# Kernel optimization log

Hardware: AMD Instinct MI355X
Metric: run time of the kernel (lower is better)

Reference implementation:

```python
import jax, jax.numpy as jnp
from jax import lax
import numpy as np

NH = 4                      # num_heads in CrossScaleCom
KS = [3, 5, 7, 9]           # per-head depthwise kernel sizes
WS = 2                      # window_size in LocalFeatureGuided
GGM_K = 7                   # guide-token generator kernel size


def _dwconv(x, w, stride, pad):
    # depthwise conv: w has shape (C, 1, k, k), feature_group_count = C
    return lax.conv_general_dilated(
        x, w, (stride, stride), [(pad, pad), (pad, pad)],
        feature_group_count=x.shape[1],
        dimension_numbers=("NCHW", "OIHW", "NCHW"))


def _forward(x, dw_w0, dw_b0, dw_w1, dw_b1, dw_w2, dw_b2, dw_w3, dw_b3,
             csc_w, csc_b, bn_gamma, bn_beta, bn_mean, bn_var,
             ggm_w, ggm_b, qkv_w, qkv_b, proj_w, proj_b):
    B, C, H, W = x.shape
    cph = C // NH
    # ---- CrossScaleCom: per-head multi-scale depthwise convs ----
    xh = x.reshape(B, NH, cph, H, W)
    dws = [(dw_w0, dw_b0), (dw_w1, dw_b1), (dw_w2, dw_b2), (dw_w3, dw_b3)]
    heads = [_dwconv(xh[:, i], w, 1, KS[i] // 2) + b[None, :, None, None]
             for i, (w, b) in enumerate(dws)]
    y = jnp.stack(heads, 1)                      # (B, NH, cph, H, W)
    y = y.transpose(0, 2, 1, 3, 4).reshape(B, C, H, W)  # channel shuffle
    y = jnp.einsum("bchw,oc->bohw", y, csc_w) + csc_b[None, :, None, None]
    Co = y.shape[1]
    # ---- LocalFeatureGuided ----
    # ggm: BatchNorm (eval) -> GELU (exact) -> depthwise conv k=7 stride=WS
    inv = bn_gamma / jnp.sqrt(bn_var + 1e-5)
    g = (y - bn_mean[None, :, None, None]) * inv[None, :, None, None] \
        + bn_beta[None, :, None, None]
    g = jax.nn.gelu(g, approximate=False)
    g = _dwconv(g, ggm_w, WS, GGM_K // 2) + ggm_b[None, :, None, None]  # (B,Co,Ho,Wo)
    Ho, Wo = H // WS, W // WS
    L = Ho * Wo
    # unfold(kernel=WS, stride=WS) -> (B, Co, WS*WS, L), torch unfold ordering
    xu = y.reshape(B, Co, Ho, WS, Wo, WS).transpose(0, 1, 3, 5, 2, 4)
    xu = xu.reshape(B, Co, WS * WS, L)
    tokens = jnp.concatenate([g.reshape(B, Co, 1, L), xu], axis=2)  # (B,Co,5,L)
    # 1x1 conv over channel dim == einsum
    qkv = jnp.einsum("bcpl,oc->bopl", tokens, qkv_w) + qkv_b[None, :, None, None]
    q, k, v = jnp.split(qkv, 3, axis=1)          # each (B, Co, 5, L)
    # tiny 5x5 attention per (batch, channel), contracting over windows L
    attn = jnp.einsum("bcpl,bcql->bcpq", q, k) / (Co ** 0.5)
    attn = jax.nn.softmax(attn, axis=-1)
    out = jnp.einsum("bcpq,bcql->bcpl", attn, v)  # (B, Co, 5, L)
    out = out[:, :, 0, :].reshape(B, Co, Ho, Wo)  # guide-token output
    out = jnp.einsum("bchw,oc->bohw", out, proj_w) + proj_b[None, :, None, None]
    return out


def setup_inputs() -> dict:
    key = jax.random.key(0)
    ks = jax.random.split(key, 16)
    B, Cin, Cout, H, W = 8, 64, 128, 224, 224
    cph = Cin // NH
    s = 0.05
    d = {"x": jax.random.normal(ks[0], (B, Cin, H, W), jnp.float32)}
    for i, kk in enumerate(KS):
        d[f"dw_w{i}"] = jax.random.normal(ks[1 + i], (cph, 1, kk, kk), jnp.float32) * s
        d[f"dw_b{i}"] = jnp.zeros((cph,), jnp.float32)
    d["csc_w"] = jax.random.normal(ks[5], (Cout, Cin), jnp.float32) * s
    d["csc_b"] = jnp.zeros((Cout,), jnp.float32)
    d["bn_gamma"] = jnp.ones((Cout,), jnp.float32)
    d["bn_beta"] = jnp.zeros((Cout,), jnp.float32)
    d["bn_mean"] = jnp.zeros((Cout,), jnp.float32)
    d["bn_var"] = jnp.ones((Cout,), jnp.float32)
    d["ggm_w"] = jax.random.normal(ks[6], (Cout, 1, GGM_K, GGM_K), jnp.float32) * s
    d["ggm_b"] = jnp.zeros((Cout,), jnp.float32)
    d["qkv_w"] = jax.random.normal(ks[7], (3 * Cout, Cout), jnp.float32) * s
    d["qkv_b"] = jnp.zeros((3 * Cout,), jnp.float32)
    d["proj_w"] = jax.random.normal(ks[8], (Cout, Cout), jnp.float32) * s
    d["proj_b"] = jnp.zeros((Cout,), jnp.float32)
    return d


def reference(x, dw_w0, dw_b0, dw_w1, dw_b1, dw_w2, dw_b2, dw_w3, dw_b3,
              csc_w, csc_b, bn_gamma, bn_beta, bn_mean, bn_var,
              ggm_w, ggm_b, qkv_w, qkv_b, proj_w, proj_b):
    return _forward(x, dw_w0, dw_b0, dw_w1, dw_b1, dw_w2, dw_b2, dw_w3, dw_b3,
                    csc_w, csc_b, bn_gamma, bn_beta, bn_mean, bn_var,
                    ggm_w, ggm_b, qkv_w, qkv_b, proj_w, proj_b)
```

## Files before the change

### kernel.cpp

```cpp
#include <hip/hip_runtime.h>

#define BB 8
#define CIN 64
#define CO 128
#define Hdim 224
#define Wdim 224
#define HWt (224*224)
#define HO 112
#define WO 112
#define Lt (112*112)

typedef unsigned short u16;
typedef short bf16x8 __attribute__((ext_vector_type(8)));
typedef float f32x4  __attribute__((ext_vector_type(4)));
#define MFMA16(a,b,c) __builtin_amdgcn_mfma_f32_16x16x32_bf16((a),(b),(c),0,0,0)

__device__ inline u16 f2bf(float f) {
    union { float f; unsigned u; } v; v.f = f;
    unsigned r = (v.u + 0x7fffu + ((v.u >> 16) & 1u)) >> 16;
    return (u16)r;
}
__device__ inline float bf2f(u16 h) {
    union { unsigned u; float f; } v; v.u = ((unsigned)h) << 16; return v.f;
}
__device__ inline float uasf(unsigned u) {
    union { unsigned u; float f; } v; v.u = u; return v.f;
}
__device__ inline float sum8bf(uint4 v) {
    return bf2f(v.x & 0xffff) + bf2f(v.x >> 16) + bf2f(v.y & 0xffff) + bf2f(v.y >> 16)
         + bf2f(v.z & 0xffff) + bf2f(v.z >> 16) + bf2f(v.w & 0xffff) + bf2f(v.w >> 16);
}

__device__ inline float gelu_fast(float x) {
    float z  = x * 0.7071067811865476f;
    float az = fabsf(z);
    float t  = __builtin_amdgcn_rcpf(fmaf(0.3275911f, az, 1.0f));
    float p  = fmaf(fmaf(fmaf(fmaf(1.061405429f, t, -1.453152027f), t,
                    1.421413741f), t, -0.284496736f), t, 0.254829592f);
    float e  = __expf(-z * z);
    float er = copysignf(1.0f - p * t * e, z);
    return 0.5f * x * (1.0f + er);
}

template<int HEAD>
__global__ __launch_bounds__(256) void dw_conv(
    const float* __restrict__ x, const float* __restrict__ w,
    const float* __restrict__ bias, u16* __restrict__ dwb)
{
    constexpr int K   = 3 + 2*HEAD;
    constexpr int PAD = HEAD + 1;
    constexpr int R   = 32 + 2*PAD;
    const int tile = blockIdx.x;
    const int c    = blockIdx.y;
    const int b    = blockIdx.z;
    const int th = (tile/7)*32, tw = (tile%7)*32;
    __shared__ float patch[R*40];
    const int tid = threadIdx.x;
    const float* xin = x + (size_t)(b*CIN + HEAD*16 + c)*HWt;
    for (int idx = tid; idx < R*40; idx += 256) {
        int r = idx / 40, cc = idx - r*40;
        int gy = th - PAD + r, gx = tw - 4 + cc;
        float v = 0.f;
        if (gy >= 0 && gy < Hdim && gx >= 0 && gx < Wdim) v = xin[gy*Wdim + gx];
        patch[idx] = v;
    }
    float wreg[K*K];
    const float* wp = w + c*K*K;
    #pragma unroll
    for (int i = 0; i < K*K; i++) wreg[i] = wp[i];
    const float bv = bias[c];
    __syncthreads();

    const int ty = tid >> 3, x0 = (tid & 7) * 4;
    float acc[4] = {bv, bv, bv, bv};
    #pragma unroll
    for (int ky = 0; ky < K; ky++) {
        float rr[12];
        *(float4*)&rr[0] = *(const float4*)&patch[(ty+ky)*40 + x0];
        *(float4*)&rr[4] = *(const float4*)&patch[(ty+ky)*40 + x0 + 4];
        *(float4*)&rr[8] = *(const float4*)&patch[(ty+ky)*40 + x0 + 8];
        #pragma unroll
        for (int kx = 0; kx < K; kx++) {
            const float wv = wreg[ky*K + kx];
            #pragma unroll
            for (int j = 0; j < 4; j++)
                acc[j] = fmaf(rr[j + kx + 4 - PAD], wv, acc[j]);
        }
    }
    const int s = c*4 + HEAD;
    u16 o4[4] = {f2bf(acc[0]), f2bf(acc[1]), f2bf(acc[2]), f2bf(acc[3])};
    *(uint2*)&dwb[(size_t)(b*CIN + s)*HWt + (th+ty)*Wdim + tw + x0] = *(uint2*)o4;
}

__global__ __launch_bounds__(256) void csc_mfma(
    const float* __restrict__ W, const float* __restrict__ bias,
    const u16* __restrict__ dwb, u16* __restrict__ y4)
{
    const int b  = blockIdx.z;
    const int p0 = blockIdx.x * 128;
    __shared__ u16 Abuf[128*72];
    __shared__ u16 Tbuf[32*132];
    const int tid = threadIdx.x;
    const int wv = tid >> 6, ln = tid & 63;
    const int mh = (wv >> 1)*64, nh = (wv & 1)*64;
    const int lm = ln & 15, kq = ln >> 4;
    for (int t = tid; t < 1024; t += 256) {
        int r = t >> 3, kk = (t & 7)*8;
        const float* src = &W[r*64 + kk];
        float4 f0 = *(const float4*)src, f1 = *(const float4*)(src+4);
        u16 tmp[8] = {f2bf(f0.x),f2bf(f0.y),f2bf(f0.z),f2bf(f0.w),
                      f2bf(f1.x),f2bf(f1.y),f2bf(f1.z),f2bf(f1.w)};
        *(uint4*)&Abuf[r*72 + kk] = *(uint4*)tmp;
    }
    const u16* Db = dwb + (size_t)b*CIN*HWt;
    f32x4 acc[4][4];
    #pragma unroll
    for (int i=0;i<4;i++)
        #pragma unroll
        for (int j=0;j<4;j++) acc[i][j] = (f32x4){0.f,0.f,0.f,0.f};

    for (int kc = 0; kc < 64; kc += 32) {
        __syncthreads();
        for (int t = tid; t < 512; t += 256) {
            int k = t >> 4, n0 = (t & 15)*8;
            *(uint4*)&Tbuf[k*132 + n0] = *(const uint4*)&Db[(size_t)(kc+k)*HWt + p0 + n0];
        }
        __syncthreads();
        bf16x8 af[4], bfr[4];
        #pragma unroll
        for (int tm=0;tm<4;tm++)
            af[tm] = *(bf16x8*)&Abuf[(mh + tm*16 + lm)*72 + kc + kq*8];
        #pragma unroll
        for (int tn=0;tn<4;tn++) {
            int n = nh + tn*16 + lm;
            #pragma unroll
            for (int j=0;j<8;j++) bfr[tn][j] = (short)Tbuf[(kq*8+j)*132 + n];
        }
        #pragma unroll
        for (int tm=0;tm<4;tm++)
            #pragma unroll
            for (int tn=0;tn<4;tn++)
                acc[tm][tn] = MFMA16(af[tm], bfr[tn], acc[tm][tn]);
    }
    #pragma unroll
    for (int tm=0;tm<4;tm++) {
        #pragma unroll
        for (int r=0;r<4;r++) {
            int o = mh + tm*16 + kq*4 + r;
            float bb = bias[o];
            #pragma unroll
            for (int tn=0;tn<4;tn++) {
                int p = p0 + nh + tn*16 + lm;
                int gy = p / 224, gx = p - gy*224;
                int w = (gy&1)*2 + (gx&1);
                y4[((size_t)(b*CO + o)*4 + w)*Lt + (gy>>1)*WO + (gx>>1)]
                    = f2bf(acc[tm][tn][r] + bb);
            }
        }
    }
}

__global__ __launch_bounds__(256) void ggm_kernel(const u16* __restrict__ y4,
    const float* __restrict__ gamma, const float* __restrict__ beta,
    const float* __restrict__ mean, const float* __restrict__ var,
    const float* __restrict__ gw, const float* __restrict__ gb,
    u16* __restrict__ gbf)
{
    const int ho0 = blockIdx.x * 16;
    const int c   = blockIdx.y;
    const int b   = blockIdx.z;
    __shared__ float patch[37*240];
    const int tid = threadIdx.x;

    const float inv = gamma[c] * rsqrtf(var[c] + 1e-5f);
    const float bsh = fmaf(-mean[c], inv, beta[c]);
    const u16* ybc = y4 + (size_t)(b*CO + c)*4*Lt;

    float wk[49];
    const float* wp = gw + c*49;
    #pragma unroll
    for (int i = 0; i < 49; i++) wk[i] = wp[i];
    const float bv = gb[c];

    for (int idx = tid; idx < 37*60; idx += 256) {
        int r = idx / 60, j = idx - r*60;
        int gy = 2*ho0 - 3 + r;
        float4 v = make_float4(0.f, 0.f, 0.f, 0.f);
        if (gy >= 0 && gy < Hdim && j >= 2 && j <= 57) {
            const u16* pe = ybc + (size_t)((gy&1)*2)*Lt + (gy>>1)*WO + (2*j - 4);
            unsigned e = *(const unsigned*)pe;
            unsigned o = *(const unsigned*)(pe + Lt);
            v.x = gelu_fast(fmaf(uasf(e << 16),         inv, bsh));
            v.y = gelu_fast(fmaf(uasf(o << 16),         inv, bsh));
            v.z = gelu_fast(fmaf(uasf(e & 0xffff0000u), inv, bsh));
            v.w = gelu_fast(fmaf(uasf(o & 0xffff0000u), inv, bsh));
        }
        *(float4*)&patch[idx*4] = v;
    }
    __syncthreads();

    if (tid < 224) {
        const int n = tid % 56;
        const int g = tid / 56;
        float acc[4][2];
        #pragma unroll
        for (int i = 0; i < 4; i++) { acc[i][0] = bv; acc[i][1] = bv; }
        #pragma unroll
        for (int rr = 0; rr < 13; rr++) {
            const float* row = &patch[(8*g + rr)*240 + 4*n + 4];
            float f[12];
            *(float4*)&f[0] = *(const float4*)&row[0];
            *(float4*)&f[4] = *(const float4*)&row[4];
            *(float4*)&f[8] = *(const float4*)&row[8];
            #pragma unroll
            for (int i = 0; i < 4; i++) {
                const int ky = rr - 2*i;
                if (ky >= 0 && ky <= 6) {
                    #pragma unroll
                    for (int kx = 0; kx < 7; kx++) {
                        const float wv = wk[ky*7 + kx];
                        acc[i][0] = fmaf(f[kx + 1], wv, acc[i][0]);
                        acc[i][1] = fmaf(f[kx + 3], wv, acc[i][1]);
                    }
                }
            }
        }
        u16* gout = gbf + (size_t)(b*CO + c)*Lt;
        #pragma unroll
        for (int i = 0; i < 4; i++) {
            u16 o2[2] = {f2bf(acc[i][0]), f2bf(acc[i][1])};
            *(unsigned*)&gout[(ho0 + 4*g + i)*WO + 2*n] = *(unsigned*)o2;
        }
    }
}

__global__ __launch_bounds__(256) void G_mfma(
    const u16* __restrict__ gbf, const u16* __restrict__ y4,
    float* __restrict__ Gpart)
{
    const int b = blockIdx.z, p = blockIdx.y, split = blockIdx.x;
    const u16* Ab = gbf + (size_t)b*CO*Lt;
    const u16* Bb; int brs;
    if (p == 0) { Bb = Ab; brs = Lt; }
    else        { Bb = y4 + ((size_t)b*CO*4 + (p-1))*Lt; brs = 4*Lt; }
    __shared__ u16 Abuf[128*72];
    __shared__ u16 Bbuf[128*72];
    const int tid = threadIdx.x;
    const int wv = tid >> 6, ln = tid & 63;
    const int mh = (wv >> 1)*64, nh = (wv & 1)*64;
    const int lm = ln & 15, kq = ln >> 4;
    f32x4 acc[4][4];
    #pragma unroll
    for (int i=0;i<4;i++)
        #pragma unroll
        for (int j=0;j<4;j++) acc[i][j] = (f32x4){0.f,0.f,0.f,0.f};

    for (int ci = split; ci < 196; ci += 16) {
        const int l0 = ci*64;
        __syncthreads();
        for (int t = tid; t < 1024; t += 256) {
            int r = t >> 3, kk = (t & 7)*8;
            *(uint4*)&Abuf[r*72 + kk] = *(const uint4*)&Ab[(size_t)r*Lt  + l0 + kk];
            *(uint4*)&Bbuf[r*72 + kk] = *(const uint4*)&Bb[(size_t)r*brs + l0 + kk];
        }
        __syncthreads();
        #pragma unroll
        for (int ks = 0; ks < 2; ks++) {
            bf16x8 af[4], bfr[4];
            #pragma unroll
            for (int tm=0;tm<4;tm++)
                af[tm]  = *(bf16x8*)&Abuf[(mh + tm*16 + lm)*72 + ks*32 + kq*8];
            #pragma unroll
            for (int tn=0;tn<4;tn++)
                bfr[tn] = *(bf16x8*)&Bbuf[(nh + tn*16 + lm)*72 + ks*32 + kq*8];
            #pragma unroll
            for (int tm=0;tm<4;tm++)
                #pragma unroll
                for (int tn=0;tn<4;tn++)
                    acc[tm][tn] = MFMA16(af[tm], bfr[tn], acc[tm][tn]);
        }
    }
    float* Go = Gpart + ((size_t)(split*40) + b*5 + p)*CO*CO;
    #pragma unroll
    for (int tm=0;tm<4;tm++)
        #pragma unroll
        for (int r=0;r<4;r++) {
            int mrow = mh + tm*16 + kq*4 + r;
            #pragma unroll
            for (int tn=0;tn<4;tn++)
                Go[mrow*CO + nh + tn*16 + lm] = acc[tm][tn][r];
        }
}

__global__ void G_reduce(const float* __restrict__ Gpart, float* __restrict__ G)
{
    const int bp = blockIdx.x;
    const int i4 = (blockIdx.y*256 + threadIdx.x)*4;
    float4 s = make_float4(0.f, 0.f, 0.f, 0.f);
    #pragma unroll
    for (int sp = 0; sp < 16; sp++) {
        float4 v = *(const float4*)&Gpart[((size_t)(sp*40) + bp)*CO*CO + i4];
        s.x += v.x; s.y += v.y; s.z += v.z; s.w += v.w;
    }
    *(float4*)&G[(size_t)bp*CO*CO + i4] = s;
}

__global__ void S_kernel(const u16* __restrict__ gbf, const u16* __restrict__ y4,
                         float* __restrict__ S)
{
    const int b = blockIdx.x >> 7, c = blockIdx.x & 127;
    const u16* gr = gbf + (size_t)(b*CO+c)*Lt;
    const u16* yr = y4  + (size_t)(b*CO+c)*4*Lt;
    float vals[5] = {0.f,0.f,0.f,0.f,0.f};
    for (int i = threadIdx.x*8; i < Lt; i += 256*8)
        vals[0] += sum8bf(*(const uint4*)&gr[i]);
    #pragma unroll
    for (int w=0; w<4; w++)
        for (int i = threadIdx.x*8; i < Lt; i += 256*8)
            vals[1+w] += sum8bf(*(const uint4*)&yr[(size_t)w*Lt + i]);
    #pragma unroll
    for (int off=32; off>0; off>>=1) {
        #pragma unroll
        for (int q=0;q<5;q++) vals[q] += __shfl_down(vals[q], off);
    }
    __shared__ float red[4][5];
    const int wid = threadIdx.x>>6, lane = threadIdx.x&63;
    if (lane==0) {
        #pragma unroll
        for (int q=0;q<5;q++) red[wid][q] = vals[q];
    }
    __syncthreads();
    if (threadIdx.x==0) {
        #pragma unroll
        for (int q=0;q<5;q++)
            S[((size_t)b*5 + q)*CO + c] = red[0][q]+red[1][q]+red[2][q]+red[3][q];
    }
}

__global__ __launch_bounds__(256) void fused_logits_kernel(
    const float* __restrict__ G, const float* __restrict__ S,
    const float* __restrict__ qkv_w, const float* __restrict__ qkv_b,
    float* __restrict__ lg)
{
    const int p = blockIdx.x, b = blockIdx.y;
    __shared__ float Wl[32*132];
    __shared__ float Al[32*132];
    __shared__ float KGl[128*128];
    const int tid = threadIdx.x;
    const int og = (tid >> 4) * 8;
    const int pg = (tid & 15) * 8;
    const float* Gp = G + (size_t)(b*5 + p)*CO*CO;
    float acc[8][8];
    #pragma unroll
    for (int i=0;i<8;i++)
        #pragma unroll
        for (int j=0;j<8;j++) acc[i][j]=0.f;

    for (int kc = 0; kc < 128; kc += 32) {
        __syncthreads();
        for (int t = tid; t < 4096; t += 256) {
            int kk = t & 31, o = t >> 5;
            Wl[kk*132 + o] = Gp[(size_t)o*CO + kc + kk];
            Al[kk*132 + o] = qkv_w[(size_t)(CO + o)*CO + kc + kk];
        }
        __syncthreads();
        #pragma unroll 4
        for (int kk = 0; kk < 32; kk++) {
            float wv[8], av[8];
            *(float4*)&wv[0] = *(const float4*)&Wl[kk*132+og];
            *(float4*)&wv[4] = *(const float4*)&Wl[kk*132+og+4];
            *(float4*)&av[0] = *(const float4*)&Al[kk*132+pg];
            *(float4*)&av[4] = *(const float4*)&Al[kk*132+pg+4];
            #pragma unroll
            for (int i=0;i<8;i++)
                #pragma unroll
                for (int j=0;j<8;j++)
                    acc[i][j] = fmaf(wv[i], av[j], acc[i][j]);
        }
    }
    #pragma unroll
    for (int i=0;i<8;i++) {
        #pragma unroll
        for (int j=0;j<8;j+=4)
            *(float4*)&KGl[(og+i)*128 + pg + j] = *(float4*)&acc[i][j];
    }
    __syncthreads();
    if (tid < 128) {
        const int c = tid;
        const float qb = qkv_b[c], kb = qkv_b[CO + c];
        const float* S0 = S + (size_t)b*5*CO;
        const float* Sp = S0 + p*CO;
        const float* qwrow = qkv_w + (size_t)c*CO;
        const float* kwrow = qkv_w + (size_t)(CO + c)*CO;
        float sq = qb * 12544.f, ks = 0.f, s = 0.f;
        for (int c2 = 0; c2 < CO; c2++) {
            sq = fmaf(qwrow[c2], S0[c2], sq);
            ks = fmaf(kwrow[c2], Sp[c2], ks);
            s  = fmaf(qwrow[c2], KGl[c2*128 + c], s);
        }
        lg[(size_t)(b*5 + p)*CO + c] = s + qb*ks + kb*sq;
    }
}

__global__ void softmax5_kernel(const float* __restrict__ lg, float* __restrict__ a)
{
    const int b = blockIdx.x, c = threadIdx.x;
    float v[5];
    #pragma unroll
    for (int p=0;p<5;p++) v[p] = lg[(size_t)(b*5 + p)*CO + c];
    const float scl = 0.08838834764831845f;
    float mx = v[0];
    #pragma unroll
    for (int p=1;p<5;p++) mx = fmaxf(mx, v[p]);
    float e[5], sum = 0.f;
    #pragma unroll
    for (int p=0;p<5;p++){ e[p] = __expf((v[p]-mx)*scl); sum += e[p]; }
    const float rs = 1.f/sum;
    #pragma unroll
    for (int p=0;p<5;p++) a[((size_t)b*CO + c)*5 + p] = e[p]*rs;
}

__global__ void F_kernel(const float* __restrict__ proj_w,
    const float* __restrict__ qkv_w, const float* __restrict__ a,
    float* __restrict__ F)
{
    const int b = blockIdx.z, p = blockIdx.y;
    const int o  = blockIdx.x*2 + (threadIdx.x>>7);
    const int cp = threadIdx.x & 127;
    const float* vw = qkv_w + 2*CO*CO;
    float s = 0.f;
    for (int c=0;c<CO;c++)
        s = fmaf(proj_w[o*CO+c] * a[((size_t)b*CO+c)*5 + p], vw[c*CO+cp], s);
    F[(((size_t)(b*5+p))*CO + o)*CO + cp] = s;
}

__global__ void bias_kernel(const float* __restrict__ proj_w,
    const float* __restrict__ proj_b, const float* __restrict__ qkv_b,
    float* __restrict__ biasout)
{
    const int o = threadIdx.x;
    const float* vb = qkv_b + 2*CO;
    float s = proj_b[o];
    for (int c=0;c<CO;c++) s = fmaf(proj_w[o*CO+c], vb[c], s);
    biasout[o] = s;
}

__global__ __launch_bounds__(256) void final_mfma(
    const float* __restrict__ F, const u16* __restrict__ gbf,
    const u16* __restrict__ y4, const float* __restrict__ biasout,
    float* __restrict__ out)
{
    const int b = blockIdx.z;
    const int p0 = blockIdx.x * 128;
    __shared__ u16 Abuf[128*40];
    __shared__ u16 Tbuf[32*132];
    const int tid = threadIdx.x;
    const int wv = tid >> 6, ln = tid & 63;
    const int mh = (wv >> 1)*64, nh = (wv & 1)*64;
    const int lm = ln & 15, kq = ln >> 4;
    f32x4 acc[4][4];
    #pragma unroll
    for (int i=0;i<4;i++)
        #pragma unroll
        for (int j=0;j<4;j++) acc[i][j] = (f32x4){0.f,0.f,0.f,0.f};

    for (int ph = 0; ph < 5; ph++) {
        const float* Fp = F + (size_t)(b*5 + ph)*CO*CO;
        const u16* Bb; int brs;
        if (ph == 0) { Bb = gbf + (size_t)b*CO*Lt; brs = Lt; }
        else         { Bb = y4 + ((size_t)b*CO*4 + (ph-1))*Lt; brs = 4*Lt; }
        for (int kc = 0; kc < CO; kc += 32) {
            __syncthreads();
            for (int t = tid; t < 512; t += 256) {
                int r = t >> 2, kk = (t & 3)*8;
                const float* src = &Fp[r*CO + kc + kk];
                float4 f0 = *(const float4*)src, f1 = *(const float4*)(src+4);
                u16 tmp[8] = {f2bf(f0.x),f2bf(f0.y),f2bf(f0.z),f2bf(f0.w),
                              f2bf(f1.x),f2bf(f1.y),f2bf(f1.z),f2bf(f1.w)};
                *(uint4*)&Abuf[r*40 + kk] = *(uint4*)tmp;
            }
            for (int t = tid; t < 512; t += 256) {
                int k = t >> 4, n0 = (t & 15)*8;
                *(uint4*)&Tbuf[k*132 + n0] = *(const uint4*)&Bb[(size_t)(kc+k)*brs + p0 + n0];
            }
            __syncthreads();
            bf16x8 af[4], bfr[4];
            #pragma unroll
            for (int tm=0;tm<4;tm++)
                af[tm] = *(bf16x8*)&Abuf[(mh + tm*16 + lm)*40 + kq*8];
            #pragma unroll
            for (int tn=0;tn<4;tn++) {
                int n = nh + tn*16 + lm;
                #pragma unroll
                for (int j=0;j<8;j++) bfr[tn][j] = (short)Tbuf[(kq*8+j)*132 + n];
            }
            #pragma unroll
            for (int tm=0;tm<4;tm++)
                #pragma unroll
                for (int tn=0;tn<4;tn++)
                    acc[tm][tn] = MFMA16(af[tm], bfr[tn], acc[tm][tn]);
        }
    }
    float* Ob = out + (size_t)b*CO*Lt;
    #pragma unroll
    for (int tm=0;tm<4;tm++) {
        #pragma unroll
        for (int r=0;r<4;r++) {
            int o = mh + tm*16 + kq*4 + r;
            float bb = biasout[o];
            #pragma unroll
            for (int tn=0;tn<4;tn++)
                Ob[(size_t)o*Lt + p0 + nh + tn*16 + lm] = acc[tm][tn][r] + bb;
        }
    }
}

extern "C" void kernel_launch(void* const* d_in, const int* in_sizes, int n_in,
                              void* d_out, int out_size, void* d_ws, size_t ws_size,
                              hipStream_t stream) {
    const float* x      = (const float*)d_in[0];
    const float* dw_w0  = (const float*)d_in[1];
    const float* dw_b0  = (const float*)d_in[2];
    const float* dw_w1  = (const float*)d_in[3];
    const float* dw_b1  = (const float*)d_in[4];
    const float* dw_w2  = (const float*)d_in[5];
    const float* dw_b2  = (const float*)d_in[6];
    const float* dw_w3  = (const float*)d_in[7];
    const float* dw_b3  = (const float*)d_in[8];
    const float* csc_w  = (const float*)d_in[9];
    const float* csc_b  = (const float*)d_in[10];
    const float* bn_g   = (const float*)d_in[11];
    const float* bn_b   = (const float*)d_in[12];
    const float* bn_m   = (const float*)d_in[13];
    const float* bn_v   = (const float*)d_in[14];
    const float* ggm_w  = (const float*)d_in[15];
    const float* ggm_b  = (const float*)d_in[16];
    const float* qkv_w  = (const float*)d_in[17];
    const float* qkv_b  = (const float*)d_in[18];
    const float* proj_w = (const float*)d_in[19];
    const float* proj_b = (const float*)d_in[20];
    float* out = (float*)d_out;

    char* ws = (char*)d_ws;
    u16*   y4  = (u16*)(ws);
    u16*   dwb = (u16*)(ws + 102760448);
    u16*   gbf = (u16*)(ws + 154140672);
    float* G   = (float*)(ws + 179830784);
    float* lgb = G  + 655360;
    float* F   = lgb + 5120;
    float* S   = F  + 655360;
    float* aw  = S  + 5120;
    float* bo  = aw + 5120;
    float* Gpart = (float*)(ws + 102760448);

    dw_conv<0><<<dim3(49, 16, 8), 256, 0, stream>>>(x, dw_w0, dw_b0, dwb);
    dw_conv<1><<<dim3(49, 16, 8), 256, 0, stream>>>(x, dw_w1, dw_b1, dwb);
    dw_conv<2><<<dim3(49, 16, 8), 256, 0, stream>>>(x, dw_w2, dw_b2, dwb);
    dw_conv<3><<<dim3(49, 16, 8), 256, 0, stream>>>(x, dw_w3, dw_b3, dwb);

    csc_mfma<<<dim3(392, 1, 8), 256, 0, stream>>>(csc_w, csc_b, dwb, y4);

    ggm_kernel<<<dim3(7, 128, 8), 256, 0, stream>>>(
        y4, bn_g, bn_b, bn_m, bn_v, ggm_w, ggm_b, gbf);

    G_mfma<<<dim3(16, 5, 8), 256, 0, stream>>>(gbf, y4, Gpart);
    G_reduce<<<dim3(40, 16), 256, 0, stream>>>(Gpart, G);

    S_kernel<<<dim3(1024), 256, 0, stream>>>(gbf, y4, S);

    fused_logits_kernel<<<dim3(5, 8), 256, 0, stream>>>(G, S, qkv_w, qkv_b, lgb);

    softmax5_kernel<<<dim3(8), 128, 0, stream>>>(lgb, aw);

    F_kernel<<<dim3(64, 5, 8), 256, 0, stream>>>(proj_w, qkv_w, aw, F);
    bias_kernel<<<dim3(1), 128, 0, stream>>>(proj_w, proj_b, qkv_b, bo);

    final_mfma<<<dim3(98, 1, 8), 256, 0, stream>>>(F, gbf, y4, bo, out);
}
```

Baseline: 626.4 us.

## Fuse token sums into ggm kernel and halve ggm row tile

Removes the separate S_kernel, which re-read gbf and y4 to compute per-channel sums. The ggm kernel now accumulates those sums while loading its patch and while producing outputs, then adds them into S with atomics. A small kernel zeroes S up front. The ggm tile also drops from 16 to 8 output rows per block, doubling the block count but raising the halo overhead (21 vs 37 rows for half the output), and atomics make the summation order nondeterministic.

```diff
diff --git a/kernel.cpp b/kernel.cpp
--- a/kernel.cpp
+++ b/kernel.cpp
@@ -26,10 +26,6 @@
 __device__ inline float uasf(unsigned u) {
     union { unsigned u; float f; } v; v.u = u; return v.f;
 }
-__device__ inline float sum8bf(uint4 v) {
-    return bf2f(v.x & 0xffff) + bf2f(v.x >> 16) + bf2f(v.y & 0xffff) + bf2f(v.y >> 16)
-         + bf2f(v.z & 0xffff) + bf2f(v.z >> 16) + bf2f(v.w & 0xffff) + bf2f(v.w >> 16);
-}
 
 __device__ inline float gelu_fast(float x) {
     float z  = x * 0.7071067811865476f;
@@ -40,6 +36,11 @@
     float e  = __expf(-z * z);
     float er = copysignf(1.0f - p * t * e, z);
     return 0.5f * x * (1.0f + er);
+}
+
+__global__ void zeroS_kernel(float* __restrict__ S) {
+    int i = blockIdx.x * 256 + threadIdx.x;
+    if (i < 5120) S[i] = 0.f;
 }
 
 template<int HEAD>
@@ -164,12 +165,13 @@
     const float* __restrict__ gamma, const float* __restrict__ beta,
     const float* __restrict__ mean, const float* __restrict__ var,
     const float* __restrict__ gw, const float* __restrict__ gb,
-    u16* __restrict__ gbf)
-{
-    const int ho0 = blockIdx.x * 16;
+    u16* __restrict__ gbf, float* __restrict__ S)
+{
+    const int ho0 = blockIdx.x * 8;
     const int c   = blockIdx.y;
     const int b   = blockIdx.z;
-    __shared__ float patch[37*240];
+    __shared__ float patch[21*240];
+    __shared__ float sred[4][5];
     const int tid = threadIdx.x;
 
     const float inv = gamma[c] * rsqrtf(var[c] + 1e-5f);
@@ -182,7 +184,8 @@
     for (int i = 0; i < 49; i++) wk[i] = wp[i];
     const float bv = gb[c];
 
-    for (int idx = tid; idx < 37*60; idx += 256) {
+    float sA[4] = {0.f, 0.f, 0.f, 0.f};
+    for (int idx = tid; idx < 21*60; idx += 256) {
         int r = idx / 60, j = idx - r*60;
         int gy = 2*ho0 - 3 + r;
         float4 v = make_float4(0.f, 0.f, 0.f, 0.f);
@@ -190,30 +193,36 @@
             const u16* pe = ybc + (size_t)((gy&1)*2)*Lt + (gy>>1)*WO + (2*j - 4);
             unsigned e = *(const unsigned*)pe;
             unsigned o = *(const unsigned*)(pe + Lt);
-            v.x = gelu_fast(fmaf(uasf(e << 16),         inv, bsh));
-            v.y = gelu_fast(fmaf(uasf(o << 16),         inv, bsh));
-            v.z = gelu_fast(fmaf(uasf(e & 0xffff0000u), inv, bsh));
-            v.w = gelu_fast(fmaf(uasf(o & 0xffff0000u), inv, bsh));
+            float e0 = uasf(e << 16), e1 = uasf(e & 0xffff0000u);
+            float o0 = uasf(o << 16), o1 = uasf(o & 0xffff0000u);
+            if (r >= 3 && r <= 18) {
+                const int rp = (gy & 1)*2;
+                sA[rp]     += e0 + e1;
+                sA[rp + 1] += o0 + o1;
+            }
+            v.x = gelu_fast(fmaf(e0, inv, bsh));
+            v.y = gelu_fast(fmaf(o0, inv, bsh));
+            v.z = gelu_fast(fmaf(e1, inv, bsh));
+            v.w = gelu_fast(fmaf(o1, inv, bsh));
         }
         *(float4*)&patch[idx*4] = v;
     }
     __syncthreads();
 
+    float gsum = 0.f;
     if (tid < 224) {
         const int n = tid % 56;
         const int g = tid / 56;
-        float acc[4][2];
-        #pragma unroll
-        for (int i = 0; i < 4; i++) { acc[i][0] = bv; acc[i][1] = bv; }
-        #pragma unroll
-        for (int rr = 0; rr < 13; rr++) {
-            const float* row = &patch[(8*g + rr)*240 + 4*n + 4];
+        float acc[2][2] = {{bv, bv}, {bv, bv}};
+        #pragma unroll
+        for (int rr = 0; rr < 9; rr++) {
+            const float* row = &patch[(4*g + rr)*240 + 4*n + 4];
             float f[12];
             *(float4*)&f[0] = *(const float4*)&row[0];
             *(float4*)&f[4] = *(const float4*)&row[4];
             *(float4*)&f[8] = *(const float4*)&row[8];
             #pragma unroll
-            for (int i = 0; i < 4; i++) {
+            for (int i = 0; i < 2; i++) {
                 const int ky = rr - 2*i;
                 if (ky >= 0 && ky <= 6) {
                     #pragma unroll
@@ -227,10 +236,28 @@
         }
         u16* gout = gbf + (size_t)(b*CO + c)*Lt;
         #pragma unroll
-        for (int i = 0; i < 4; i++) {
+        for (int i = 0; i < 2; i++) {
             u16 o2[2] = {f2bf(acc[i][0]), f2bf(acc[i][1])};
-            *(unsigned*)&gout[(ho0 + 4*g + i)*WO + 2*n] = *(unsigned*)o2;
-        }
+            *(unsigned*)&gout[(ho0 + 2*g + i)*WO + 2*n] = *(unsigned*)o2;
+        }
+        gsum = acc[0][0] + acc[0][1] + acc[1][0] + acc[1][1];
+    }
+
+    float red[5] = {gsum, sA[0], sA[1], sA[2], sA[3]};
+    #pragma unroll
+    for (int off = 32; off > 0; off >>= 1) {
+        #pragma unroll
+        for (int q = 0; q < 5; q++) red[q] += __shfl_down(red[q], off);
+    }
+    const int wid = tid >> 6, lane = tid & 63;
+    if (lane == 0) {
+        #pragma unroll
+        for (int q = 0; q < 5; q++) sred[wid][q] = red[q];
+    }
+    __syncthreads();
+    if (tid < 5) {
+        atomicAdd(&S[((size_t)b*5 + tid)*CO + c],
+                  sred[0][tid] + sred[1][tid] + sred[2][tid] + sred[3][tid]);
     }
 }
 
@@ -303,38 +330,6 @@
         s.x += v.x; s.y += v.y; s.z += v.z; s.w += v.w;
     }
     *(float4*)&G[(size_t)bp*CO*CO + i4] = s;
-}
-
-__global__ void S_kernel(const u16* __restrict__ gbf, const u16* __restrict__ y4,
-                         float* __restrict__ S)
-{
-    const int b = blockIdx.x >> 7, c = blockIdx.x & 127;
-    const u16* gr = gbf + (size_t)(b*CO+c)*Lt;
-    const u16* yr = y4  + (size_t)(b*CO+c)*4*Lt;
-    float vals[5] = {0.f,0.f,0.f,0.f,0.f};
-    for (int i = threadIdx.x*8; i < Lt; i += 256*8)
-        vals[0] += sum8bf(*(const uint4*)&gr[i]);
-    #pragma unroll
-    for (int w=0; w<4; w++)
-        for (int i = threadIdx.x*8; i < Lt; i += 256*8)
-            vals[1+w] += sum8bf(*(const uint4*)&yr[(size_t)w*Lt + i]);
-    #pragma unroll
-    for (int off=32; off>0; off>>=1) {
-        #pragma unroll
-        for (int q=0;q<5;q++) vals[q] += __shfl_down(vals[q], off);
-    }
-    __shared__ float red[4][5];
-    const int wid = threadIdx.x>>6, lane = threadIdx.x&63;
-    if (lane==0) {
-        #pragma unroll
-        for (int q=0;q<5;q++) red[wid][q] = vals[q];
-    }
-    __syncthreads();
-    if (threadIdx.x==0) {
-        #pragma unroll
-        for (int q=0;q<5;q++)
-            S[((size_t)b*5 + q)*CO + c] = red[0][q]+red[1][q]+red[2][q]+red[3][q];
-    }
 }
 
 __global__ __launch_bounds__(256) void fused_logits_kernel(
@@ -553,6 +548,8 @@
     float* bo  = aw + 5120;
     float* Gpart = (float*)(ws + 102760448);
 
+    zeroS_kernel<<<dim3(20), 256, 0, stream>>>(S);
+
     dw_conv<0><<<dim3(49, 16, 8), 256, 0, stream>>>(x, dw_w0, dw_b0, dwb);
     dw_conv<1><<<dim3(49, 16, 8), 256, 0, stream>>>(x, dw_w1, dw_b1, dwb);
     dw_conv<2><<<dim3(49, 16, 8), 256, 0, stream>>>(x, dw_w2, dw_b2, dwb);
@@ -560,14 +557,12 @@
 
     csc_mfma<<<dim3(392, 1, 8), 256, 0, stream>>>(csc_w, csc_b, dwb, y4);
 
-    ggm_kernel<<<dim3(7, 128, 8), 256, 0, stream>>>(
-        y4, bn_g, bn_b, bn_m, bn_v, ggm_w, ggm_b, gbf);
+    ggm_kernel<<<dim3(14, 128, 8), 256, 0, stream>>>(
+        y4, bn_g, bn_b, bn_m, bn_v, ggm_w, ggm_b, gbf, S);
 
     G_mfma<<<dim3(16, 5, 8), 256, 0, stream>>>(gbf, y4, Gpart);
     G_reduce<<<dim3(40, 16), 256, 0, stream>>>(Gpart, G);
 
-    S_kernel<<<dim3(1024), 256, 0, stream>>>(gbf, y4, S);
-
     fused_logits_kernel<<<dim3(5, 8), 256, 0, stream>>>(G, S, qkv_w, qkv_b, lgb);
 
     softmax5_kernel<<<dim3(8), 128, 0, stream>>>(lgb, aw);
```

Result: no change. 615.4 us (-1.8%).

## Fuse column sums into G MFMA, widen ggm blocks, store F as bf16

Applied to the files above, without the earlier changes.

Removes the separate S_kernel reduction pass. Column sums are computed inside G_mfma by multiplying a ones-row A fragment with the already-staged B tiles, and the per-split partials are reduced in G_reduce. This avoids re-reading gbf and y4 from global memory. The ggm depthwise kernel now runs 512 threads per block, each computing 2 output rows instead of 4, for more parallelism. F_kernel writes bf16 directly so final_mfma loads it without converting in the inner loop, at the cost of the extra MFMA work on one wave pair in G_mfma.

```diff
diff --git a/kernel.cpp b/kernel.cpp
--- a/kernel.cpp
+++ b/kernel.cpp
@@ -25,10 +25,6 @@
 }
 __device__ inline float uasf(unsigned u) {
     union { unsigned u; float f; } v; v.u = u; return v.f;
-}
-__device__ inline float sum8bf(uint4 v) {
-    return bf2f(v.x & 0xffff) + bf2f(v.x >> 16) + bf2f(v.y & 0xffff) + bf2f(v.y >> 16)
-         + bf2f(v.z & 0xffff) + bf2f(v.z >> 16) + bf2f(v.w & 0xffff) + bf2f(v.w >> 16);
 }
 
 __device__ inline float gelu_fast(float x) {
@@ -160,7 +156,7 @@
     }
 }
 
-__global__ __launch_bounds__(256) void ggm_kernel(const u16* __restrict__ y4,
+__global__ __launch_bounds__(512) void ggm_kernel(const u16* __restrict__ y4,
     const float* __restrict__ gamma, const float* __restrict__ beta,
     const float* __restrict__ mean, const float* __restrict__ var,
     const float* __restrict__ gw, const float* __restrict__ gb,
@@ -182,7 +178,7 @@
     for (int i = 0; i < 49; i++) wk[i] = wp[i];
     const float bv = gb[c];
 
-    for (int idx = tid; idx < 37*60; idx += 256) {
+    for (int idx = tid; idx < 37*60; idx += 512) {
         int r = idx / 60, j = idx - r*60;
         int gy = 2*ho0 - 3 + r;
         float4 v = make_float4(0.f, 0.f, 0.f, 0.f);
@@ -199,21 +195,19 @@
     }
     __syncthreads();
 
-    if (tid < 224) {
+    if (tid < 448) {
         const int n = tid % 56;
         const int g = tid / 56;
-        float acc[4][2];
-        #pragma unroll
-        for (int i = 0; i < 4; i++) { acc[i][0] = bv; acc[i][1] = bv; }
-        #pragma unroll
-        for (int rr = 0; rr < 13; rr++) {
-            const float* row = &patch[(8*g + rr)*240 + 4*n + 4];
+        float acc[2][2] = {{bv, bv}, {bv, bv}};
+        #pragma unroll
+        for (int rr = 0; rr < 9; rr++) {
+            const float* row = &patch[(4*g + rr)*240 + 4*n + 4];
             float f[12];
             *(float4*)&f[0] = *(const float4*)&row[0];
             *(float4*)&f[4] = *(const float4*)&row[4];
             *(float4*)&f[8] = *(const float4*)&row[8];
             #pragma unroll
-            for (int i = 0; i < 4; i++) {
+            for (int i = 0; i < 2; i++) {
                 const int ky = rr - 2*i;
                 if (ky >= 0 && ky <= 6) {
                     #pragma unroll
@@ -227,16 +221,16 @@
         }
         u16* gout = gbf + (size_t)(b*CO + c)*Lt;
         #pragma unroll
-        for (int i = 0; i < 4; i++) {
+        for (int i = 0; i < 2; i++) {
             u16 o2[2] = {f2bf(acc[i][0]), f2bf(acc[i][1])};
-            *(unsigned*)&gout[(ho0 + 4*g + i)*WO + 2*n] = *(unsigned*)o2;
+            *(unsigned*)&gout[(ho0 + 2*g + i)*WO + 2*n] = *(unsigned*)o2;
         }
     }
 }
 
 __global__ __launch_bounds__(256) void G_mfma(
     const u16* __restrict__ gbf, const u16* __restrict__ y4,
-    float* __restrict__ Gpart)
+    float* __restrict__ Gpart, float* __restrict__ Spart)
 {
     const int b = blockIdx.z, p = blockIdx.y, split = blockIdx.x;
     const u16* Ab = gbf + (size_t)b*CO*Lt;
@@ -254,6 +248,13 @@
     for (int i=0;i<4;i++)
         #pragma unroll
         for (int j=0;j<4;j++) acc[i][j] = (f32x4){0.f,0.f,0.f,0.f};
+    bf16x8 af_s;
+    #pragma unroll
+    for (int j=0;j<8;j++) af_s[j] = (lm == 0) ? (short)0x3F80 : (short)0;
+    f32x4 acc_s[4];
+    #pragma unroll
+    for (int j=0;j<4;j++) acc_s[j] = (f32x4){0.f,0.f,0.f,0.f};
+    const bool sWave = (mh == 0);
 
     for (int ci = split; ci < 196; ci += 16) {
         const int l0 = ci*64;
@@ -278,6 +279,11 @@
                 #pragma unroll
                 for (int tn=0;tn<4;tn++)
                     acc[tm][tn] = MFMA16(af[tm], bfr[tn], acc[tm][tn]);
+            if (sWave) {
+                #pragma unroll
+                for (int tn=0;tn<4;tn++)
+                    acc_s[tn] = MFMA16(af_s, bfr[tn], acc_s[tn]);
+            }
         }
     }
     float* Go = Gpart + ((size_t)(split*40) + b*5 + p)*CO*CO;
@@ -290,9 +296,17 @@
             for (int tn=0;tn<4;tn++)
                 Go[mrow*CO + nh + tn*16 + lm] = acc[tm][tn][r];
         }
-}
-
-__global__ void G_reduce(const float* __restrict__ Gpart, float* __restrict__ G)
+    if (sWave && kq == 0) {
+        float* So = Spart + ((size_t)(split*40) + b*5 + p)*CO;
+        #pragma unroll
+        for (int tn=0;tn<4;tn++)
+            So[nh + tn*16 + lm] = acc_s[tn][0];
+    }
+}
+
+__global__ void G_reduce(const float* __restrict__ Gpart,
+                         const float* __restrict__ Spart,
+                         float* __restrict__ G, float* __restrict__ S)
 {
     const int bp = blockIdx.x;
     const int i4 = (blockIdx.y*256 + threadIdx.x)*4;
@@ -303,37 +317,12 @@
         s.x += v.x; s.y += v.y; s.z += v.z; s.w += v.w;
     }
     *(float4*)&G[(size_t)bp*CO*CO + i4] = s;
-}
-
-__global__ void S_kernel(const u16* __restrict__ gbf, const u16* __restrict__ y4,
-                         float* __restrict__ S)
-{
-    const int b = blockIdx.x >> 7, c = blockIdx.x & 127;
-    const u16* gr = gbf + (size_t)(b*CO+c)*Lt;
-    const u16* yr = y4  + (size_t)(b*CO+c)*4*Lt;
-    float vals[5] = {0.f,0.f,0.f,0.f,0.f};
-    for (int i = threadIdx.x*8; i < Lt; i += 256*8)
-        vals[0] += sum8bf(*(const uint4*)&gr[i]);
-    #pragma unroll
-    for (int w=0; w<4; w++)
-        for (int i = threadIdx.x*8; i < Lt; i += 256*8)
-            vals[1+w] += sum8bf(*(const uint4*)&yr[(size_t)w*Lt + i]);
-    #pragma unroll
-    for (int off=32; off>0; off>>=1) {
-        #pragma unroll
-        for (int q=0;q<5;q++) vals[q] += __shfl_down(vals[q], off);
-    }
-    __shared__ float red[4][5];
-    const int wid = threadIdx.x>>6, lane = threadIdx.x&63;
-    if (lane==0) {
-        #pragma unroll
-        for (int q=0;q<5;q++) red[wid][q] = vals[q];
-    }
-    __syncthreads();
-    if (threadIdx.x==0) {
-        #pragma unroll
-        for (int q=0;q<5;q++)
-            S[((size_t)b*5 + q)*CO + c] = red[0][q]+red[1][q]+red[2][q]+red[3][q];
+    if (blockIdx.y == 0 && threadIdx.x < CO) {
+        float ss = 0.f;
+        #pragma unroll
+        for (int sp = 0; sp < 16; sp++)
+            ss += Spart[((size_t)(sp*40) + bp)*CO + threadIdx.x];
+        S[(size_t)bp*CO + threadIdx.x] = ss;
     }
 }
 
@@ -422,7 +411,7 @@
 
 __global__ void F_kernel(const float* __restrict__ proj_w,
     const float* __restrict__ qkv_w, const float* __restrict__ a,
-    float* __restrict__ F)
+    u16* __restrict__ Fb)
 {
     const int b = blockIdx.z, p = blockIdx.y;
     const int o  = blockIdx.x*2 + (threadIdx.x>>7);
@@ -431,7 +420,7 @@
     float s = 0.f;
     for (int c=0;c<CO;c++)
         s = fmaf(proj_w[o*CO+c] * a[((size_t)b*CO+c)*5 + p], vw[c*CO+cp], s);
-    F[(((size_t)(b*5+p))*CO + o)*CO + cp] = s;
+    Fb[(((size_t)(b*5+p))*CO + o)*CO + cp] = f2bf(s);
 }
 
 __global__ void bias_kernel(const float* __restrict__ proj_w,
@@ -446,7 +435,7 @@
 }
 
 __global__ __launch_bounds__(256) void final_mfma(
-    const float* __restrict__ F, const u16* __restrict__ gbf,
+    const u16* __restrict__ Fb, const u16* __restrict__ gbf,
     const u16* __restrict__ y4, const float* __restrict__ biasout,
     float* __restrict__ out)
 {
@@ -465,7 +454,7 @@
         for (int j=0;j<4;j++) acc[i][j] = (f32x4){0.f,0.f,0.f,0.f};
 
     for (int ph = 0; ph < 5; ph++) {
-        const float* Fp = F + (size_t)(b*5 + ph)*CO*CO;
+        const u16* Fp = Fb + (size_t)(b*5 + ph)*CO*CO;
         const u16* Bb; int brs;
         if (ph == 0) { Bb = gbf + (size_t)b*CO*Lt; brs = Lt; }
         else         { Bb = y4 + ((size_t)b*CO*4 + (ph-1))*Lt; brs = 4*Lt; }
@@ -473,11 +462,7 @@
             __syncthreads();
             for (int t = tid; t < 512; t += 256) {
                 int r = t >> 2, kk = (t & 3)*8;
-                const float* src = &Fp[r*CO + kc + kk];
-                float4 f0 = *(const float4*)src, f1 = *(const float4*)(src+4);
-                u16 tmp[8] = {f2bf(f0.x),f2bf(f0.y),f2bf(f0.z),f2bf(f0.w),
-                              f2bf(f1.x),f2bf(f1.y),f2bf(f1.z),f2bf(f1.w)};
-                *(uint4*)&Abuf[r*40 + kk] = *(uint4*)tmp;
+                *(uint4*)&Abuf[r*40 + kk] = *(const uint4*)&Fp[r*CO + kc + kk];
             }
             for (int t = tid; t < 512; t += 256) {
                 int k = t >> 4, n0 = (t & 15)*8;
@@ -546,12 +531,13 @@
     u16*   dwb = (u16*)(ws + 102760448);
     u16*   gbf = (u16*)(ws + 154140672);
     float* G   = (float*)(ws + 179830784);
-    float* lgb = G  + 655360;
-    float* F   = lgb + 5120;
-    float* S   = F  + 655360;
-    float* aw  = S  + 5120;
-    float* bo  = aw + 5120;
+    float* lgb = (float*)(ws + 182452224);
+    u16*   Fb  = (u16*)  (ws + 182472704);
+    float* S   = (float*)(ws + 183783424);
+    float* aw  = (float*)(ws + 183803904);
+    float* bo  = (float*)(ws + 183824384);
     float* Gpart = (float*)(ws + 102760448);
+    float* Spart = (float*)(ws + 144703488);
 
     dw_conv<0><<<dim3(49, 16, 8), 256, 0, stream>>>(x, dw_w0, dw_b0, dwb);
     dw_conv<1><<<dim3(49, 16, 8), 256, 0, stream>>>(x, dw_w1, dw_b1, dwb);
@@ -560,20 +546,18 @@
 
     csc_mfma<<<dim3(392, 1, 8), 256, 0, stream>>>(csc_w, csc_b, dwb, y4);
 
-    ggm_kernel<<<dim3(7, 128, 8), 256, 0, stream>>>(
+    ggm_kernel<<<dim3(7, 128, 8), 512, 0, stream>>>(
         y4, bn_g, bn_b, bn_m, bn_v, ggm_w, ggm_b, gbf);
 
-    G_mfma<<<dim3(16, 5, 8), 256, 0, stream>>>(gbf, y4, Gpart);
-    G_reduce<<<dim3(40, 16), 256, 0, stream>>>(Gpart, G);
-
-    S_kernel<<<dim3(1024), 256, 0, stream>>>(gbf, y4, S);
+    G_mfma<<<dim3(16, 5, 8), 256, 0, stream>>>(gbf, y4, Gpart, Spart);
+    G_reduce<<<dim3(40, 16), 256, 0, stream>>>(Gpart, Spart, G, S);
 
     fused_logits_kernel<<<dim3(5, 8), 256, 0, stream>>>(G, S, qkv_w, qkv_b, lgb);
 
     softmax5_kernel<<<dim3(8), 128, 0, stream>>>(lgb, aw);
 
-    F_kernel<<<dim3(64, 5, 8), 256, 0, stream>>>(proj_w, qkv_w, aw, F);
+    F_kernel<<<dim3(64, 5, 8), 256, 0, stream>>>(proj_w, qkv_w, aw, Fb);
     bias_kernel<<<dim3(1), 128, 0, stream>>>(proj_w, proj_b, qkv_b, bo);
 
-    final_mfma<<<dim3(98, 1, 8), 256, 0, stream>>>(F, gbf, y4, bo, out);
-}
+    final_mfma<<<dim3(98, 1, 8), 256, 0, stream>>>(Fb, gbf, y4, bo, out);
+}
```

New measurement: 617.7 us. No clear change (-1.4%).
